# Optimization experiments

Measured on AMD Instinct MI355X. Metric: run time of the kernel, lower is better.

The kernel has to match this reference:

```python
import jax, jax.numpy as jnp
import numpy as np

B = 32; H = 56; W = 56; C = 384; WS = 7; SHIFT = 3; NH = 12; HID = 1536; RANK = 192
N = WS * WS
NWIN = (H // WS) * (W // WS)


def _rel_index():
    coords = np.stack(np.meshgrid(np.arange(WS), np.arange(WS), indexing='ij')).reshape(2, -1)
    rel = (coords[:, :, None] - coords[:, None, :]).transpose(1, 2, 0)
    rel[..., 0] += WS - 1
    rel[..., 1] += WS - 1
    rel[..., 0] *= 2 * WS - 1
    return jnp.asarray(rel.sum(-1).reshape(-1))  # (N*N,) int


def _attn_mask():
    img = np.zeros((H, W))
    cnt = 0
    sls = (slice(0, -WS), slice(-WS, -SHIFT), slice(-SHIFT, None))
    for hs in sls:
        for ws_ in sls:
            img[hs, ws_] = cnt
            cnt += 1
    mw = img.reshape(H // WS, WS, W // WS, WS).transpose(0, 2, 1, 3).reshape(-1, N)
    am = mw[:, None, :] - mw[:, :, None]
    return jnp.asarray(np.where(am != 0, -100.0, 0.0).astype(np.float32))  # (nW,N,N)


REL_IDX = _rel_index()
ATTN_MASK = _attn_mask()


def _ln(x, g, b):
    m = x.mean(-1, keepdims=True)
    v = ((x - m) ** 2).mean(-1, keepdims=True)
    return (x - m) / jnp.sqrt(v + 1e-5) * g + b


def _flin(x, v, u, b):
    # FactorizedLinear: x @ V^T @ U^T + b
    return (x @ v.T) @ u.T + b


def setup_inputs() -> dict:
    key = jax.random.key(0)
    ks = jax.random.split(key, 12)
    def n(k, shape, s):
        return jax.random.normal(k, shape, jnp.float32) * s
    return {
        'x': jax.random.normal(ks[0], (B, H * W, C), jnp.float32),
        'norm1_g': jnp.ones((C,), jnp.float32), 'norm1_b': jnp.zeros((C,), jnp.float32),
        'rpb_table': n(ks[1], ((2 * WS - 1) ** 2, NH), 0.02),
        'qkv_v': n(ks[2], (RANK, C), 0.05), 'qkv_u': n(ks[3], (3 * C, RANK), 0.05),
        'qkv_b': jnp.zeros((3 * C,), jnp.float32),
        'proj_v': n(ks[4], (RANK, C), 0.05), 'proj_u': n(ks[5], (C, RANK), 0.05),
        'proj_b': jnp.zeros((C,), jnp.float32),
        'norm2_g': jnp.ones((C,), jnp.float32), 'norm2_b': jnp.zeros((C,), jnp.float32),
        'fc1_v': n(ks[6], (RANK, C), 0.05), 'fc1_u': n(ks[7], (HID, RANK), 0.05),
        'fc1_b': jnp.zeros((HID,), jnp.float32),
        'fc2_v': n(ks[8], (RANK, HID), 0.05), 'fc2_u': n(ks[9], (C, RANK), 0.05),
        'fc2_b': jnp.zeros((C,), jnp.float32),
    }


def reference(x, norm1_g, norm1_b, rpb_table, qkv_v, qkv_u, qkv_b,
              proj_v, proj_u, proj_b, norm2_g, norm2_b,
              fc1_v, fc1_u, fc1_b, fc2_v, fc2_u, fc2_b):
    hd = C // NH
    scale = hd ** -0.5
    shortcut = x
    y = _ln(x, norm1_g, norm1_b).reshape(B, H, W, C)
    y = jnp.roll(y, (-SHIFT, -SHIFT), axis=(1, 2))  # cyclic shift
    # window partition -> (B*nW, N, C)
    y = y.reshape(B, H // WS, WS, W // WS, WS, C).transpose(0, 1, 3, 2, 4, 5).reshape(-1, N, C)
    qkv = _flin(y, qkv_v, qkv_u, qkv_b).reshape(-1, N, 3, NH, hd).transpose(2, 0, 3, 1, 4)
    q, k, v = qkv[0] * scale, qkv[1], qkv[2]  # (B*nW, NH, N, hd)
    attn = jnp.einsum('bhnd,bhmd->bhnm', q, k)
    rpb = rpb_table[REL_IDX].reshape(N, N, NH).transpose(2, 0, 1)  # (NH,N,N)
    attn = attn + rpb[None]
    attn = attn.reshape(B, NWIN, NH, N, N) + ATTN_MASK[None, :, None]
    attn = jax.nn.softmax(attn, axis=-1).reshape(-1, NH, N, N)
    o = jnp.einsum('bhnm,bhmd->bhnd', attn, v).transpose(0, 2, 1, 3).reshape(-1, N, C)
    o = _flin(o, proj_v, proj_u, proj_b)
    # window reverse + reverse shift
    o = o.reshape(B, H // WS, W // WS, WS, WS, C).transpose(0, 1, 3, 2, 4, 5).reshape(B, H, W, C)
    o = jnp.roll(o, (SHIFT, SHIFT), axis=(1, 2)).reshape(B, H * W, C)
    x = shortcut + o
    z = _ln(x, norm2_g, norm2_b)
    z = jax.nn.gelu(_flin(z, fc1_v, fc1_u, fc1_b), approximate=False)
    z = _flin(z, fc2_v, fc2_u, fc2_b)
    return x + z
```

## Files before the change

kernel.cpp:

```cpp
#include <hip/hip_runtime.h>
#include <hip/hip_bf16.h>

using bf16 = __hip_bfloat16;
typedef __bf16 bf16x8 __attribute__((ext_vector_type(8)));
typedef __bf16 bf16x4v __attribute__((ext_vector_type(4)));
typedef float f32x4 __attribute__((ext_vector_type(4)));

#define MROWS 100352

__device__ __forceinline__ void async16(void* l, const void* g) {
    void* gg = const_cast<void*>(g);
    __builtin_amdgcn_global_load_lds((__attribute__((address_space(1))) void*)gg,
                                     (__attribute__((address_space(3))) void*)l, 16, 0, 0);
}

__device__ __forceinline__ float gelu_f(float x) {
    float u = 0.7978845608028654f * (x + 0.044715f * x * x * x);
    float e = __expf(2.0f * u);
    float t = 1.0f - 2.0f / (e + 1.0f);
    return 0.5f * x * (1.0f + t);
}

struct Cvt8 { const float* s[8]; bf16* d[8]; int n[8]; };

__global__ __launch_bounds__(256) void cvt8_k(Cvt8 c) {
    int seg = blockIdx.y;
    int i4 = (blockIdx.x * 256 + threadIdx.x) * 4;
    if (i4 < c.n[seg]) {
        float4 v = *(const float4*)(c.s[seg] + i4);
        bf16* d = c.d[seg] + i4;
        d[0] = __float2bfloat16(v.x);
        d[1] = __float2bfloat16(v.y);
        d[2] = __float2bfloat16(v.z);
        d[3] = __float2bfloat16(v.w);
    }
}

__global__ __launch_bounds__(256) void bias_pre_k(const float* __restrict__ rpbt,
                                                  float* __restrict__ biasf) {
    int wt = blockIdx.x / 12, h = blockIdx.x % 12;
    int t = threadIdx.x;
    int lane = t >> 2, tb = t & 3;
    int hi = lane >> 4, lo = lane & 15;
    int m = tb * 16 + lo;
    bool bH = (wt & 2) != 0, bW = (wt & 1) != 0;
    float* outb = biasf + (size_t)blockIdx.x * 4096;
    int mm = m < 49 ? m : 0;
    int i2 = mm / 7, j2 = mm % 7;
    int rm = (bH ? (i2 < 4 ? 1 : 2) : 0) * 3 + (bW ? (j2 < 4 ? 1 : 2) : 0);
#pragma unroll
    for (int ta = 0; ta < 4; ++ta) {
#pragma unroll
        for (int j = 0; j < 4; ++j) {
            int n = ta * 16 + hi * 4 + j;
            float v;
            if (n < 49 && m < 49) {
                int i1 = n / 7, j1 = n % 7;
                int rn = (bH ? (i1 < 4 ? 1 : 2) : 0) * 3 + (bW ? (j1 < 4 ? 1 : 2) : 0);
                v = rpbt[((i1 - i2 + 6) * 13 + (j1 - j2 + 6)) * 12 + h];
                if (rn != rm) v -= 100.0f;
            } else {
                v = -1e30f;
            }
            outb[(ta * 4 + j) * 256 + t] = v;
        }
    }
}

__global__ __launch_bounds__(256) void ln1_window_k(const float* __restrict__ x,
                                                    const float* __restrict__ g,
                                                    const float* __restrict__ bta,
                                                    bf16* __restrict__ ywin) {
    int wrow = blockIdx.x * 4 + (threadIdx.x >> 6);
    int lane = threadIdx.x & 63;
    int tok = wrow % 49, win = wrow / 49;
    int i = tok / 7, j = tok % 7;
    int wwi = win & 7, whi = (win >> 3) & 7, bi = win >> 6;
    int hs = (whi * 7 + i + 3) % 56;
    int ws_ = (wwi * 7 + j + 3) % 56;
    const float* xr = x + ((size_t)bi * 3136 + (size_t)hs * 56 + ws_) * 384;
    float v[6]; float s = 0.f, s2 = 0.f;
#pragma unroll
    for (int u = 0; u < 6; ++u) { float t = xr[lane + 64 * u]; v[u] = t; s += t; s2 += t * t; }
#pragma unroll
    for (int d = 1; d < 64; d <<= 1) { s += __shfl_xor(s, d); s2 += __shfl_xor(s2, d); }
    float mean = s * (1.0f / 384.0f);
    float var = s2 * (1.0f / 384.0f) - mean * mean;
    float rstd = rsqrtf(var + 1e-5f);
    bf16* yr = ywin + (size_t)wrow * 384;
#pragma unroll
    for (int u = 0; u < 6; ++u) {
        int c = lane + 64 * u;
        yr[c] = __float2bfloat16((v[u] - mean) * rstd * g[c] + bta[c]);
    }
}

__global__ __launch_bounds__(256) void resid_ln2_k(const float* __restrict__ x,
                                                   const bf16* __restrict__ proj,
                                                   const float* __restrict__ g,
                                                   const float* __restrict__ bta,
                                                   float* __restrict__ x2,
                                                   bf16* __restrict__ z) {
    int row = blockIdx.x * 4 + (threadIdx.x >> 6);
    int lane = threadIdx.x & 63;
    int bi = row / 3136; int hw = row % 3136;
    int h = hw / 56, w = hw % 56;
    int h2 = (h + 53) % 56, w2 = (w + 53) % 56;
    int prow = ((bi * 8 + h2 / 7) * 8 + w2 / 7) * 49 + (h2 % 7) * 7 + (w2 % 7);
    const float* xr = x + (size_t)row * 384;
    const bf16* pr = proj + (size_t)prow * 384;
    float* x2r = x2 + (size_t)row * 384;
    float v[6]; float s = 0.f, s2 = 0.f;
#pragma unroll
    for (int u = 0; u < 6; ++u) {
        int c = lane + 64 * u;
        float t = xr[c] + __bfloat162float(pr[c]);
        v[u] = t; s += t; s2 += t * t;
        x2r[c] = t;
    }
#pragma unroll
    for (int d = 1; d < 64; d <<= 1) { s += __shfl_xor(s, d); s2 += __shfl_xor(s2, d); }
    float mean = s * (1.0f / 384.0f);
    float var = s2 * (1.0f / 384.0f) - mean * mean;
    float rstd = rsqrtf(var + 1e-5f);
    bf16* zr = z + (size_t)row * 384;
#pragma unroll
    for (int u = 0; u < 6; ++u) {
        int c = lane + 64 * u;
        zr[c] = __float2bfloat16((v[u] - mean) * rstd * g[c] + bta[c]);
    }
}

__global__ __launch_bounds__(256) void attn_mfma_k(const bf16* __restrict__ qkv,
                                                   const float* __restrict__ biasf,
                                                   bf16* __restrict__ o) {
    __shared__ __align__(16) __bf16 vt_s[4][32 * 72];
    __shared__ __align__(16) __bf16 p_s[4][32 * 72];
    const int win = blockIdx.x;
    const int r = blockIdx.y;
    const int wave = threadIdx.x >> 6, lane = threadIdx.x & 63;
    const int lo = lane & 15, hi = lane >> 4;
    const int whi = (win >> 3) & 7, wwi = win & 7;
    const int wt = ((whi == 7) ? 2 : 0) + ((wwi == 7) ? 1 : 0);
    __bf16* vt_w = vt_s[wave];
    __bf16* p_w = p_s[wave];
    const int h = r * 4 + wave;
    const bf16* qbase = qkv + (size_t)win * 49 * 1152 + h * 32;
    const float* btile = biasf + (size_t)(wt * 12 + h) * 4096;
    bf16x8 zf = {};

    {
        int m = lane;
        bf16x8 vrow[4];
#pragma unroll
        for (int d8 = 0; d8 < 4; ++d8)
            vrow[d8] = (m < 49) ? *(const bf16x8*)(qbase + (size_t)m * 1152 + 768 + d8 * 8) : zf;
#pragma unroll
        for (int d8 = 0; d8 < 4; ++d8)
#pragma unroll
            for (int e = 0; e < 8; ++e)
                vt_w[(d8 * 8 + e) * 72 + m] = vrow[d8][e];
    }
    bf16x8 aq[4], bk[4];
    const int kq = hi * 8;
#pragma unroll
    for (int ta = 0; ta < 4; ++ta) {
        int n = ta * 16 + lo;
        aq[ta] = (n < 49) ? *(const bf16x8*)(qbase + (size_t)n * 1152 + kq) : zf;
        bk[ta] = (n < 49) ? *(const bf16x8*)(qbase + (size_t)n * 1152 + 384 + kq) : zf;
    }
    f32x4 acc[4][4] = {};
#pragma unroll
    for (int ta = 0; ta < 4; ++ta)
#pragma unroll
        for (int tb = 0; tb < 4; ++tb)
            acc[ta][tb] = __builtin_amdgcn_mfma_f32_16x16x32_bf16(aq[ta], bk[tb], acc[ta][tb], 0, 0, 0);
#pragma unroll
    for (int ta = 0; ta < 4; ++ta) {
#pragma unroll
        for (int j = 0; j < 4; ++j) {
            float4 b4 = *(const float4*)(btile + (ta * 4 + j) * 256 + lane * 4);
            acc[ta][0][j] = fmaf(acc[ta][0][j], 0.17677669529663687f, b4.x);
            acc[ta][1][j] = fmaf(acc[ta][1][j], 0.17677669529663687f, b4.y);
            acc[ta][2][j] = fmaf(acc[ta][2][j], 0.17677669529663687f, b4.z);
            acc[ta][3][j] = fmaf(acc[ta][3][j], 0.17677669529663687f, b4.w);
        }
    }
    bf16x8 vb[2][2];
#pragma unroll
    for (int kb = 0; kb < 2; ++kb)
#pragma unroll
        for (int tb = 0; tb < 2; ++tb)
            vb[kb][tb] = *(const bf16x8*)(vt_w + (tb * 16 + lo) * 72 + kb * 32 + hi * 8);

    f32x4 oacc[4][2] = {};
#pragma unroll
    for (int half = 0; half < 2; ++half) {
#pragma unroll
        for (int tq = 0; tq < 2; ++tq) {
            int ta = half * 2 + tq;
#pragma unroll
            for (int j = 0; j < 4; ++j) {
                float mx = fmaxf(fmaxf(acc[ta][0][j], acc[ta][1][j]),
                                 fmaxf(acc[ta][2][j], acc[ta][3][j]));
                mx = fmaxf(mx, __shfl_xor(mx, 1));
                mx = fmaxf(mx, __shfl_xor(mx, 2));
                mx = fmaxf(mx, __shfl_xor(mx, 4));
                mx = fmaxf(mx, __shfl_xor(mx, 8));
                float e0 = __expf(acc[ta][0][j] - mx);
                float e1 = __expf(acc[ta][1][j] - mx);
                float e2 = __expf(acc[ta][2][j] - mx);
                float e3 = __expf(acc[ta][3][j] - mx);
                float sm = e0 + e1 + e2 + e3;
                sm += __shfl_xor(sm, 1);
                sm += __shfl_xor(sm, 2);
                sm += __shfl_xor(sm, 4);
                sm += __shfl_xor(sm, 8);
                float inv = 1.0f / sm;
                int nl = tq * 16 + hi * 4 + j;
                p_w[nl * 72 + lo]      = (__bf16)(e0 * inv);
                p_w[nl * 72 + 16 + lo] = (__bf16)(e1 * inv);
                p_w[nl * 72 + 32 + lo] = (__bf16)(e2 * inv);
                p_w[nl * 72 + 48 + lo] = (__bf16)(e3 * inv);
            }
        }
#pragma unroll
        for (int kb = 0; kb < 2; ++kb) {
#pragma unroll
            for (int tq = 0; tq < 2; ++tq) {
                bf16x8 pa = *(const bf16x8*)(p_w + (tq * 16 + lo) * 72 + kb * 32 + hi * 8);
#pragma unroll
                for (int tb = 0; tb < 2; ++tb)
                    oacc[half * 2 + tq][tb] =
                        __builtin_amdgcn_mfma_f32_16x16x32_bf16(pa, vb[kb][tb], oacc[half * 2 + tq][tb], 0, 0, 0);
            }
        }
    }
    bf16* obase = o + (size_t)win * 49 * 384 + h * 32;
#pragma unroll
    for (int ta = 0; ta < 4; ++ta) {
#pragma unroll
        for (int j = 0; j < 4; ++j) {
            int n = ta * 16 + hi * 4 + j;
            if (n < 49) {
#pragma unroll
                for (int tb = 0; tb < 2; ++tb)
                    obase[(size_t)n * 384 + tb * 16 + lo] = __float2bfloat16(oacc[ta][tb][j]);
            }
        }
    }
}

template <int K, int N, int WN, int EPI>
__global__ __launch_bounds__(WN * 128, 8 - WN) void gemm_bt(const bf16* __restrict__ A,
                                                            const bf16* __restrict__ W,
                                                            const float* __restrict__ bias,
                                                            void* __restrict__ Cout) {
    constexpr int T = WN * 128;
    constexpr int BN = WN * 32;
    __shared__ __align__(16) bf16 lds_a[128 * 64];
    __shared__ __align__(16) bf16 lds_b[BN * 64];
    const int t = threadIdx.x;
    const int wave = t >> 6, lane = t & 63;
    const int gdx = gridDim.x;
    int flat = blockIdx.y * gdx + blockIdx.x;
    int q = (gdx * gridDim.y) >> 3;
    int work = (flat & 7) * q + (flat >> 3);
    const int n0 = (work % gdx) * BN, m0 = (work / gdx) * 128;
    const int wm = wave / WN, wn = wave % WN;
    const int fr = lane & 15, hi = lane >> 4;
    const int srow = t >> 3;
    const int gslot = (t & 7) ^ (srow & 7);
    const bf16* abase = A + (size_t)(m0 + srow) * K + gslot * 8;
    const bf16* bbase = W + (size_t)(n0 + srow) * K + gslot * 8;
    char* la = (char*)lds_a + t * 16;
    char* lb = (char*)lds_b + t * 16;
    const int fp = fr & 7;
    const char* ra0 = (const char*)lds_a + (wm * 64 + fr) * 128 + (hi ^ fp) * 16;
    const char* ra1 = (const char*)lds_a + (wm * 64 + fr) * 128 + ((4 + hi) ^ fp) * 16;
    const char* rb0 = (const char*)lds_b + (wn * 32 + fr) * 128 + (hi ^ fp) * 16;
    const char* rb1 = (const char*)lds_b + (wn * 32 + fr) * 128 + ((4 + hi) ^ fp) * 16;
    f32x4 acc[4][2] = {};
#pragma unroll
    for (int kt = 0; kt < K; kt += 64) {
        if (kt > 0) __syncthreads();
#pragma unroll
        for (int i = 0; i < 1024 / T; ++i)
            async16(la + i * T * 16, abase + (size_t)i * (T >> 3) * K + kt);
#pragma unroll
        for (int i = 0; i < BN * 8 / T; ++i)
            async16(lb + i * T * 16, bbase + (size_t)i * (T >> 3) * K + kt);
        __syncthreads();
        bf16x8 af[4], bfr[2];
#pragma unroll
        for (int mi = 0; mi < 4; ++mi) af[mi] = *(const bf16x8*)(ra0 + mi * 2048);
#pragma unroll
        for (int ni = 0; ni < 2; ++ni) bfr[ni] = *(const bf16x8*)(rb0 + ni * 2048);
#pragma unroll
        for (int mi = 0; mi < 4; ++mi)
#pragma unroll
            for (int ni = 0; ni < 2; ++ni)
                acc[mi][ni] = __builtin_amdgcn_mfma_f32_16x16x32_bf16(bfr[ni], af[mi], acc[mi][ni], 0, 0, 0);
#pragma unroll
        for (int mi = 0; mi < 4; ++mi) af[mi] = *(const bf16x8*)(ra1 + mi * 2048);
#pragma unroll
        for (int ni = 0; ni < 2; ++ni) bfr[ni] = *(const bf16x8*)(rb1 + ni * 2048);
#pragma unroll
        for (int mi = 0; mi < 4; ++mi)
#pragma unroll
            for (int ni = 0; ni < 2; ++ni)
                acc[mi][ni] = __builtin_amdgcn_mfma_f32_16x16x32_bf16(bfr[ni], af[mi], acc[mi][ni], 0, 0, 0);
    }
    const int rq4 = hi * 4;
    const int ncol = n0 + wn * 32 + rq4;
    const size_t cbase = (size_t)(m0 + wm * 64 + fr) * N + ncol;
    const float* pb = bias ? bias + ncol : nullptr;
#pragma unroll
    for (int mi = 0; mi < 4; ++mi) {
#pragma unroll
        for (int ni = 0; ni < 2; ++ni) {
            float v0 = acc[mi][ni][0], v1 = acc[mi][ni][1];
            float v2 = acc[mi][ni][2], v3 = acc[mi][ni][3];
            if (pb) {
                float4 b4 = *(const float4*)(pb + ni * 16);
                v0 += b4.x; v1 += b4.y; v2 += b4.z; v3 += b4.w;
            }
            if (EPI == 1) { v0 = gelu_f(v0); v1 = gelu_f(v1); v2 = gelu_f(v2); v3 = gelu_f(v3); }
            if (EPI == 2) {
                float4* p = (float4*)((float*)Cout + cbase + (size_t)mi * 16 * N + ni * 16);
                float4 o = *p;
                o.x += v0; o.y += v1; o.z += v2; o.w += v3;
                *p = o;
            } else {
                bf16x4v st = { (__bf16)v0, (__bf16)v1, (__bf16)v2, (__bf16)v3 };
                *(bf16x4v*)((bf16*)Cout + cbase + (size_t)mi * 16 * N + ni * 16) = st;
            }
        }
    }
}

extern "C" void kernel_launch(void* const* d_in, const int* in_sizes, int n_in,
                              void* d_out, int out_size, void* d_ws, size_t ws_size,
                              hipStream_t stream) {
    const float* x      = (const float*)d_in[0];
    const float* n1g    = (const float*)d_in[1];
    const float* n1b    = (const float*)d_in[2];
    const float* rpbt   = (const float*)d_in[3];
    const float* qkv_v  = (const float*)d_in[4];
    const float* qkv_u  = (const float*)d_in[5];
    const float* qkv_b  = (const float*)d_in[6];
    const float* proj_v = (const float*)d_in[7];
    const float* proj_u = (const float*)d_in[8];
    const float* proj_b = (const float*)d_in[9];
    const float* n2g    = (const float*)d_in[10];
    const float* n2b    = (const float*)d_in[11];
    const float* fc1_v  = (const float*)d_in[12];
    const float* fc1_u  = (const float*)d_in[13];
    const float* fc1_b  = (const float*)d_in[14];
    const float* fc2_v  = (const float*)d_in[15];
    const float* fc2_u  = (const float*)d_in[16];
    const float* fc2_b  = (const float*)d_in[17];

    char* ws = (char*)d_ws;
    bf16* wb = (bf16*)ws;
    bf16* w_qkv_v  = wb;
    bf16* w_qkv_u  = wb + 73728;
    bf16* w_proj_v = wb + 294912;
    bf16* w_proj_u = wb + 368640;
    bf16* w_fc1_v  = wb + 442368;
    bf16* w_fc1_u  = wb + 516096;
    bf16* w_fc2_v  = wb + 811008;
    bf16* w_fc2_u  = wb + 1105920;
    float* biasf   = (float*)(ws + 3145728);
    size_t off = (size_t)4 << 20;
    bf16* R1 = (bf16*)(ws + off); off += (size_t)MROWS * 1536 * 2;
    bf16* R2 = (bf16*)(ws + off); off += (size_t)MROWS * 384 * 2;
    bf16* R3 = (bf16*)(ws + off);
    float* out = (float*)d_out;

    Cvt8 c;
    c.s[0] = qkv_v;  c.d[0] = w_qkv_v;  c.n[0] = 73728;
    c.s[1] = qkv_u;  c.d[1] = w_qkv_u;  c.n[1] = 221184;
    c.s[2] = proj_v; c.d[2] = w_proj_v; c.n[2] = 73728;
    c.s[3] = proj_u; c.d[3] = w_proj_u; c.n[3] = 73728;
    c.s[4] = fc1_v;  c.d[4] = w_fc1_v;  c.n[4] = 73728;
    c.s[5] = fc1_u;  c.d[5] = w_fc1_u;  c.n[5] = 294912;
    c.s[6] = fc2_v;  c.d[6] = w_fc2_v;  c.n[6] = 294912;
    c.s[7] = fc2_u;  c.d[7] = w_fc2_u;  c.n[7] = 73728;
    cvt8_k<<<dim3(288, 8), 256, 0, stream>>>(c);
    bias_pre_k<<<48, 256, 0, stream>>>(rpbt, biasf);

    ln1_window_k<<<MROWS / 4, 256, 0, stream>>>(x, n1g, n1b, R2);
    gemm_bt<384, 192, 2, 0><<<dim3(3, 784), 256, 0, stream>>>(R2, w_qkv_v, nullptr, R3);
    gemm_bt<192, 1152, 4, 0><<<dim3(9, 784), 512, 0, stream>>>(R3, w_qkv_u, qkv_b, R1);
    attn_mfma_k<<<dim3(2048, 3), 256, 0, stream>>>(R1, biasf, R2);
    gemm_bt<384, 192, 2, 0><<<dim3(3, 784), 256, 0, stream>>>(R2, w_proj_v, nullptr, R3);
    gemm_bt<192, 384, 4, 0><<<dim3(3, 784), 512, 0, stream>>>(R3, w_proj_u, proj_b, R1);
    resid_ln2_k<<<MROWS / 4, 256, 0, stream>>>(x, R1, n2g, n2b, out, R2);
    gemm_bt<384, 192, 2, 0><<<dim3(3, 784), 256, 0, stream>>>(R2, w_fc1_v, nullptr, R3);
    gemm_bt<192, 1536, 4, 1><<<dim3(12, 784), 512, 0, stream>>>(R3, w_fc1_u, fc1_b, R1);
    gemm_bt<1536, 192, 2, 0><<<dim3(3, 784), 256, 0, stream>>>(R1, w_fc2_v, nullptr, R3);
    gemm_bt<192, 384, 4, 2><<<dim3(3, 784), 512, 0, stream>>>(R3, w_fc2_u, fc2_b, out);
}
```

Before: 841.8 us.

## Merge proj low-rank weights, add direct-load B GEMM, cheaper gelu/softmax reciprocals

Precomputes the proj U·V product on device so the projection becomes a single K=384 GEMM instead of two chained low-rank GEMMs, removing one launch and an intermediate round trip. Adds a gemm_bu variant for the wide-N U-side GEMMs that loads B fragments straight from global memory into registers and stages only A in LDS. It also rewrites gelu in sigmoid form with a hardware reciprocal and uses rcp in the softmax normalisation. The merged projection does more FLOPs than the factorized pair, and the direct B loads depend on cache hits.

```diff
diff --git a/kernel.cpp b/kernel.cpp
--- a/kernel.cpp
+++ b/kernel.cpp
@@ -15,10 +15,9 @@
 }
 
 __device__ __forceinline__ float gelu_f(float x) {
-    float u = 0.7978845608028654f * (x + 0.044715f * x * x * x);
-    float e = __expf(2.0f * u);
-    float t = 1.0f - 2.0f / (e + 1.0f);
-    return 0.5f * x * (1.0f + t);
+    float u = x * fmaf(0.044715f * x, x, 1.0f);
+    float e = __expf(-1.5957691216057308f * u);
+    return x * __builtin_amdgcn_rcpf(1.0f + e);
 }
 
 struct Cvt8 { const float* s[8]; bf16* d[8]; int n[8]; };
@@ -34,6 +33,16 @@
         d[2] = __float2bfloat16(v.z);
         d[3] = __float2bfloat16(v.w);
     }
+}
+
+__global__ __launch_bounds__(384) void wmerge_k(const float* __restrict__ u,
+                                                const float* __restrict__ v,
+                                                bf16* __restrict__ wm) {
+    int o = blockIdx.x, i = threadIdx.x;
+    const float* ur = u + o * 192;
+    float acc = 0.f;
+    for (int r = 0; r < 192; ++r) acc = fmaf(ur[r], v[r * 384 + i], acc);
+    wm[o * 384 + i] = __float2bfloat16(acc);
 }
 
 __global__ __launch_bounds__(256) void bias_pre_k(const float* __restrict__ rpbt,
@@ -216,7 +225,7 @@
                 sm += __shfl_xor(sm, 2);
                 sm += __shfl_xor(sm, 4);
                 sm += __shfl_xor(sm, 8);
-                float inv = 1.0f / sm;
+                float inv = __builtin_amdgcn_rcpf(sm);
                 int nl = tq * 16 + hi * 4 + j;
                 p_w[nl * 72 + lo]      = (__bf16)(e0 * inv);
                 p_w[nl * 72 + 16 + lo] = (__bf16)(e1 * inv);
@@ -251,23 +260,21 @@
     }
 }
 
-template <int K, int N, int WN, int EPI>
-__global__ __launch_bounds__(WN * 128, 8 - WN) void gemm_bt(const bf16* __restrict__ A,
-                                                            const bf16* __restrict__ W,
-                                                            const float* __restrict__ bias,
-                                                            void* __restrict__ Cout) {
-    constexpr int T = WN * 128;
-    constexpr int BN = WN * 32;
+template <int K, int N, int EPI>
+__global__ __launch_bounds__(256, 6) void gemm_bt(const bf16* __restrict__ A,
+                                                  const bf16* __restrict__ W,
+                                                  const float* __restrict__ bias,
+                                                  void* __restrict__ Cout) {
     __shared__ __align__(16) bf16 lds_a[128 * 64];
-    __shared__ __align__(16) bf16 lds_b[BN * 64];
+    __shared__ __align__(16) bf16 lds_b[64 * 64];
     const int t = threadIdx.x;
     const int wave = t >> 6, lane = t & 63;
     const int gdx = gridDim.x;
     int flat = blockIdx.y * gdx + blockIdx.x;
     int q = (gdx * gridDim.y) >> 3;
     int work = (flat & 7) * q + (flat >> 3);
-    const int n0 = (work % gdx) * BN, m0 = (work / gdx) * 128;
-    const int wm = wave / WN, wn = wave % WN;
+    const int n0 = (work % gdx) * 64, m0 = (work / gdx) * 128;
+    const int wm = wave >> 1, wn = wave & 1;
     const int fr = lane & 15, hi = lane >> 4;
     const int srow = t >> 3;
     const int gslot = (t & 7) ^ (srow & 7);
@@ -285,11 +292,11 @@
     for (int kt = 0; kt < K; kt += 64) {
         if (kt > 0) __syncthreads();
 #pragma unroll
-        for (int i = 0; i < 1024 / T; ++i)
-            async16(la + i * T * 16, abase + (size_t)i * (T >> 3) * K + kt);
-#pragma unroll
-        for (int i = 0; i < BN * 8 / T; ++i)
-            async16(lb + i * T * 16, bbase + (size_t)i * (T >> 3) * K + kt);
+        for (int i = 0; i < 4; ++i)
+            async16(la + i * 4096, abase + (size_t)i * 32 * K + kt);
+#pragma unroll
+        for (int i = 0; i < 2; ++i)
+            async16(lb + i * 4096, bbase + (size_t)i * 32 * K + kt);
         __syncthreads();
         bf16x8 af[4], bfr[2];
 #pragma unroll
@@ -310,6 +317,84 @@
 #pragma unroll
             for (int ni = 0; ni < 2; ++ni)
                 acc[mi][ni] = __builtin_amdgcn_mfma_f32_16x16x32_bf16(bfr[ni], af[mi], acc[mi][ni], 0, 0, 0);
+    }
+    const int rq4 = hi * 4;
+    const int ncol = n0 + wn * 32 + rq4;
+    const size_t cbase = (size_t)(m0 + wm * 64 + fr) * N + ncol;
+    const float* pb = bias ? bias + ncol : nullptr;
+#pragma unroll
+    for (int mi = 0; mi < 4; ++mi) {
+#pragma unroll
+        for (int ni = 0; ni < 2; ++ni) {
+            float v0 = acc[mi][ni][0], v1 = acc[mi][ni][1];
+            float v2 = acc[mi][ni][2], v3 = acc[mi][ni][3];
+            if (pb) {
+                float4 b4 = *(const float4*)(pb + ni * 16);
+                v0 += b4.x; v1 += b4.y; v2 += b4.z; v3 += b4.w;
+            }
+            if (EPI == 1) { v0 = gelu_f(v0); v1 = gelu_f(v1); v2 = gelu_f(v2); v3 = gelu_f(v3); }
+            if (EPI == 2) {
+                float4* p = (float4*)((float*)Cout + cbase + (size_t)mi * 16 * N + ni * 16);
+                float4 o = *p;
+                o.x += v0; o.y += v1; o.z += v2; o.w += v3;
+                *p = o;
+            } else {
+                bf16x4v st = { (__bf16)v0, (__bf16)v1, (__bf16)v2, (__bf16)v3 };
+                *(bf16x4v*)((bf16*)Cout + cbase + (size_t)mi * 16 * N + ni * 16) = st;
+            }
+        }
+    }
+}
+
+template <int K, int N, int EPI>
+__global__ __launch_bounds__(512, 6) void gemm_bu(const bf16* __restrict__ A,
+                                                  const bf16* __restrict__ W,
+                                                  const float* __restrict__ bias,
+                                                  void* __restrict__ Cout) {
+    __shared__ __align__(16) bf16 lds_a[128 * 64];
+    const int t = threadIdx.x;
+    const int wave = t >> 6, lane = t & 63;
+    const int gdx = gridDim.x;
+    int flat = blockIdx.y * gdx + blockIdx.x;
+    int q = (gdx * gridDim.y) >> 3;
+    int work = (flat & 7) * q + (flat >> 3);
+    const int n0 = (work % gdx) * 128, m0 = (work / gdx) * 128;
+    const int wm = wave >> 2, wn = wave & 3;
+    const int fr = lane & 15, hi = lane >> 4;
+    const int srow = t >> 3;
+    const int gslot = (t & 7) ^ (srow & 7);
+    const bf16* abase = A + (size_t)(m0 + srow) * K + gslot * 8;
+    char* la = (char*)lds_a + t * 16;
+    const bf16* wbase = W + (size_t)(n0 + wn * 32 + fr) * K + hi * 8;
+    const int fp = fr & 7;
+    const char* ra0 = (const char*)lds_a + (wm * 64 + fr) * 128 + (hi ^ fp) * 16;
+    const char* ra1 = (const char*)lds_a + (wm * 64 + fr) * 128 + ((4 + hi) ^ fp) * 16;
+    f32x4 acc[4][2] = {};
+#pragma unroll 1
+    for (int kt = 0; kt < K; kt += 64) {
+        bf16x8 b00 = *(const bf16x8*)(wbase + kt);
+        bf16x8 b01 = *(const bf16x8*)(wbase + (size_t)16 * K + kt);
+        bf16x8 b10 = *(const bf16x8*)(wbase + kt + 32);
+        bf16x8 b11 = *(const bf16x8*)(wbase + (size_t)16 * K + kt + 32);
+        if (kt > 0) __syncthreads();
+        async16(la, abase + kt);
+        async16(la + 8192, abase + (size_t)64 * K + kt);
+        __syncthreads();
+        bf16x8 af[4];
+#pragma unroll
+        for (int mi = 0; mi < 4; ++mi) af[mi] = *(const bf16x8*)(ra0 + mi * 2048);
+#pragma unroll
+        for (int mi = 0; mi < 4; ++mi) {
+            acc[mi][0] = __builtin_amdgcn_mfma_f32_16x16x32_bf16(b00, af[mi], acc[mi][0], 0, 0, 0);
+            acc[mi][1] = __builtin_amdgcn_mfma_f32_16x16x32_bf16(b01, af[mi], acc[mi][1], 0, 0, 0);
+        }
+#pragma unroll
+        for (int mi = 0; mi < 4; ++mi) af[mi] = *(const bf16x8*)(ra1 + mi * 2048);
+#pragma unroll
+        for (int mi = 0; mi < 4; ++mi) {
+            acc[mi][0] = __builtin_amdgcn_mfma_f32_16x16x32_bf16(b10, af[mi], acc[mi][0], 0, 0, 0);
+            acc[mi][1] = __builtin_amdgcn_mfma_f32_16x16x32_bf16(b11, af[mi], acc[mi][1], 0, 0, 0);
+        }
     }
     const int rq4 = hi * 4;
     const int ncol = n0 + wn * 32 + rq4;
@@ -371,6 +456,7 @@
     bf16* w_fc1_u  = wb + 516096;
     bf16* w_fc2_v  = wb + 811008;
     bf16* w_fc2_u  = wb + 1105920;
+    bf16* w_proj_m = wb + 1179648;
     float* biasf   = (float*)(ws + 3145728);
     size_t off = (size_t)4 << 20;
     bf16* R1 = (bf16*)(ws + off); off += (size_t)MROWS * 1536 * 2;
@@ -389,16 +475,16 @@
     c.s[7] = fc2_u;  c.d[7] = w_fc2_u;  c.n[7] = 73728;
     cvt8_k<<<dim3(288, 8), 256, 0, stream>>>(c);
     bias_pre_k<<<48, 256, 0, stream>>>(rpbt, biasf);
+    wmerge_k<<<384, 384, 0, stream>>>(proj_u, proj_v, w_proj_m);
 
     ln1_window_k<<<MROWS / 4, 256, 0, stream>>>(x, n1g, n1b, R2);
-    gemm_bt<384, 192, 2, 0><<<dim3(3, 784), 256, 0, stream>>>(R2, w_qkv_v, nullptr, R3);
-    gemm_bt<192, 1152, 4, 0><<<dim3(9, 784), 512, 0, stream>>>(R3, w_qkv_u, qkv_b, R1);
+    gemm_bt<384, 192, 0><<<dim3(3, 784), 256, 0, stream>>>(R2, w_qkv_v, nullptr, R3);
+    gemm_bu<192, 1152, 0><<<dim3(9, 784), 512, 0, stream>>>(R3, w_qkv_u, qkv_b, R1);
     attn_mfma_k<<<dim3(2048, 3), 256, 0, stream>>>(R1, biasf, R2);
-    gemm_bt<384, 192, 2, 0><<<dim3(3, 784), 256, 0, stream>>>(R2, w_proj_v, nullptr, R3);
-    gemm_bt<192, 384, 4, 0><<<dim3(3, 784), 512, 0, stream>>>(R3, w_proj_u, proj_b, R1);
+    gemm_bu<384, 384, 0><<<dim3(3, 784), 512, 0, stream>>>(R2, w_proj_m, proj_b, R1);
     resid_ln2_k<<<MROWS / 4, 256, 0, stream>>>(x, R1, n2g, n2b, out, R2);
-    gemm_bt<384, 192, 2, 0><<<dim3(3, 784), 256, 0, stream>>>(R2, w_fc1_v, nullptr, R3);
-    gemm_bt<192, 1536, 4, 1><<<dim3(12, 784), 512, 0, stream>>>(R3, w_fc1_u, fc1_b, R1);
-    gemm_bt<1536, 192, 2, 0><<<dim3(3, 784), 256, 0, stream>>>(R1, w_fc2_v, nullptr, R3);
-    gemm_bt<192, 384, 4, 2><<<dim3(3, 784), 512, 0, stream>>>(R3, w_fc2_u, fc2_b, out);
-}
+    gemm_bt<384, 192, 0><<<dim3(3, 784), 256, 0, stream>>>(R2, w_fc1_v, nullptr, R3);
+    gemm_bu<192, 1536, 1><<<dim3(12, 784), 512, 0, stream>>>(R3, w_fc1_u, fc1_b, R1);
+    gemm_bt<1536, 192, 0><<<dim3(3, 784), 256, 0, stream>>>(R1, w_fc2_v, nullptr, R3);
+    gemm_bu<192, 384, 2><<<dim3(3, 784), 512, 0, stream>>>(R3, w_fc2_u, fc2_b, out);
+}
```

Measured after the change: 933.4 us. 10.9% more time.

## Fuse MLP fc1_u+GELU+fc2_v on-chip and premerge projection factors

Applied to the files above, without the earlier changes.

Adds mlp_mid_k, which computes the fc1 up-projection, bias and GELU in 128-column chunks kept in LDS and immediately feeds them into the fc2 down-projection, so the 1536-wide hidden activation is never written to or read from global memory. It also premultiplies proj_u·proj_v into a single 384x384 weight so the attention output projection becomes one GEMM instead of two. GELU is rewritten in sigmoid form with a hardware reciprocal, and the softmax divide uses rcp. The risks are lower occupancy from the large LDS footprint in the fused kernel, more FLOPs in the merged projection, and reduced precision from the approximate reciprocal.

```diff
diff --git a/kernel.cpp b/kernel.cpp
--- a/kernel.cpp
+++ b/kernel.cpp
@@ -15,10 +15,9 @@
 }
 
 __device__ __forceinline__ float gelu_f(float x) {
-    float u = 0.7978845608028654f * (x + 0.044715f * x * x * x);
-    float e = __expf(2.0f * u);
-    float t = 1.0f - 2.0f / (e + 1.0f);
-    return 0.5f * x * (1.0f + t);
+    float u = x * fmaf(0.044715f * x, x, 1.0f);
+    float e = __expf(-1.5957691216057308f * u);
+    return x * __builtin_amdgcn_rcpf(1.0f + e);
 }
 
 struct Cvt8 { const float* s[8]; bf16* d[8]; int n[8]; };
@@ -34,6 +33,16 @@
         d[2] = __float2bfloat16(v.z);
         d[3] = __float2bfloat16(v.w);
     }
+}
+
+__global__ __launch_bounds__(384) void wmerge_k(const float* __restrict__ u,
+                                                const float* __restrict__ v,
+                                                bf16* __restrict__ wm) {
+    int o = blockIdx.x, i = threadIdx.x;
+    const float* ur = u + o * 192;
+    float acc = 0.f;
+    for (int r = 0; r < 192; ++r) acc = fmaf(ur[r], v[r * 384 + i], acc);
+    wm[o * 384 + i] = __float2bfloat16(acc);
 }
 
 __global__ __launch_bounds__(256) void bias_pre_k(const float* __restrict__ rpbt,
@@ -216,7 +225,7 @@
                 sm += __shfl_xor(sm, 2);
                 sm += __shfl_xor(sm, 4);
                 sm += __shfl_xor(sm, 8);
-                float inv = 1.0f / sm;
+                float inv = __builtin_amdgcn_rcpf(sm);
                 int nl = tq * 16 + hi * 4 + j;
                 p_w[nl * 72 + lo]      = (__bf16)(e0 * inv);
                 p_w[nl * 72 + 16 + lo] = (__bf16)(e1 * inv);
@@ -339,6 +348,100 @@
     }
 }
 
+__global__ __launch_bounds__(512, 4) void mlp_mid_k(const bf16* __restrict__ A,
+                                                    const bf16* __restrict__ U,
+                                                    const bf16* __restrict__ V2,
+                                                    const float* __restrict__ b1,
+                                                    bf16* __restrict__ Cout) {
+    __shared__ __align__(16) bf16 lds_a[128 * 192];
+    __shared__ __align__(16) bf16 lds_h[128 * 128];
+    const int t = threadIdx.x;
+    const int wave = t >> 6, lane = t & 63;
+    const int wm = wave >> 2, wn = wave & 3;
+    const int fr = lane & 15, hi = lane >> 4;
+    const int fp = fr & 7;
+    const int m0 = blockIdx.x * 128;
+#pragma unroll
+    for (int i = 0; i < 6; ++i) {
+        int u = i * 512 + t;
+        int row = u / 24, slot = u % 24;
+        int gslot = slot ^ (row & 7);
+        async16((char*)lds_a + u * 16, A + (size_t)(m0 + row) * 192 + gslot * 8);
+    }
+    __syncthreads();
+
+    f32x4 acc2[4][3] = {};
+    const int rowm = wm * 64;
+    const bf16* ub = U + (size_t)(wn * 32 + fr) * 192 + hi * 8;
+    const bf16* vb = V2 + (size_t)(wn * 48 + fr) * 1536 + hi * 8;
+
+    for (int hc = 0; hc < 12; ++hc) {
+        f32x4 acc1[4][2] = {};
+#pragma unroll
+        for (int kk = 0; kk < 6; ++kk) {
+            bf16x8 af[4], bu[2];
+#pragma unroll
+            for (int mi = 0; mi < 4; ++mi) {
+                int row = rowm + mi * 16 + fr;
+                af[mi] = *(const bf16x8*)((const char*)lds_a + row * 384 + ((kk * 4 + hi) ^ fp) * 16);
+            }
+#pragma unroll
+            for (int nn = 0; nn < 2; ++nn)
+                bu[nn] = *(const bf16x8*)(ub + (size_t)(hc * 128 + nn * 16) * 192 + kk * 32);
+#pragma unroll
+            for (int mi = 0; mi < 4; ++mi)
+#pragma unroll
+                for (int nn = 0; nn < 2; ++nn)
+                    acc1[mi][nn] = __builtin_amdgcn_mfma_f32_16x16x32_bf16(bu[nn], af[mi], acc1[mi][nn], 0, 0, 0);
+        }
+        if (hc > 0) __syncthreads();
+#pragma unroll
+        for (int nn = 0; nn < 2; ++nn) {
+            float4 b4 = *(const float4*)(b1 + hc * 128 + wn * 32 + nn * 16 + hi * 4);
+#pragma unroll
+            for (int mi = 0; mi < 4; ++mi) {
+                int mrow = rowm + mi * 16 + fr;
+                float v0 = gelu_f(acc1[mi][nn][0] + b4.x);
+                float v1 = gelu_f(acc1[mi][nn][1] + b4.y);
+                float v2 = gelu_f(acc1[mi][nn][2] + b4.z);
+                float v3 = gelu_f(acc1[mi][nn][3] + b4.w);
+                bf16x4v st = { (__bf16)v0, (__bf16)v1, (__bf16)v2, (__bf16)v3 };
+                int hb = (wn * 64 + nn * 32 + hi * 8) ^ ((mrow & 7) << 4);
+                *(bf16x4v*)((char*)lds_h + mrow * 256 + hb) = st;
+            }
+        }
+        __syncthreads();
+#pragma unroll
+        for (int kk = 0; kk < 4; ++kk) {
+            bf16x8 af2[4], bv[3];
+#pragma unroll
+            for (int mi = 0; mi < 4; ++mi) {
+                int mrow = rowm + mi * 16 + fr;
+                int kb = (kk * 64 + hi * 16) ^ ((mrow & 7) << 4);
+                af2[mi] = *(const bf16x8*)((const char*)lds_h + mrow * 256 + kb);
+            }
+#pragma unroll
+            for (int tn = 0; tn < 3; ++tn)
+                bv[tn] = *(const bf16x8*)(vb + (size_t)(tn * 16) * 1536 + hc * 128 + kk * 32);
+#pragma unroll
+            for (int mi = 0; mi < 4; ++mi)
+#pragma unroll
+                for (int tn = 0; tn < 3; ++tn)
+                    acc2[mi][tn] = __builtin_amdgcn_mfma_f32_16x16x32_bf16(bv[tn], af2[mi], acc2[mi][tn], 0, 0, 0);
+        }
+    }
+    const size_t cbase = (size_t)(m0 + rowm + fr) * 192 + wn * 48 + hi * 4;
+#pragma unroll
+    for (int mi = 0; mi < 4; ++mi) {
+#pragma unroll
+        for (int tn = 0; tn < 3; ++tn) {
+            bf16x4v st = { (__bf16)acc2[mi][tn][0], (__bf16)acc2[mi][tn][1],
+                           (__bf16)acc2[mi][tn][2], (__bf16)acc2[mi][tn][3] };
+            *(bf16x4v*)(Cout + cbase + (size_t)mi * 16 * 192 + tn * 16) = st;
+        }
+    }
+}
+
 extern "C" void kernel_launch(void* const* d_in, const int* in_sizes, int n_in,
                               void* d_out, int out_size, void* d_ws, size_t ws_size,
                               hipStream_t stream) {
@@ -371,6 +474,7 @@
     bf16* w_fc1_u  = wb + 516096;
     bf16* w_fc2_v  = wb + 811008;
     bf16* w_fc2_u  = wb + 1105920;
+    bf16* w_proj_m = wb + 1179648;
     float* biasf   = (float*)(ws + 3145728);
     size_t off = (size_t)4 << 20;
     bf16* R1 = (bf16*)(ws + off); off += (size_t)MROWS * 1536 * 2;
@@ -389,16 +493,15 @@
     c.s[7] = fc2_u;  c.d[7] = w_fc2_u;  c.n[7] = 73728;
     cvt8_k<<<dim3(288, 8), 256, 0, stream>>>(c);
     bias_pre_k<<<48, 256, 0, stream>>>(rpbt, biasf);
+    wmerge_k<<<384, 384, 0, stream>>>(proj_u, proj_v, w_proj_m);
 
     ln1_window_k<<<MROWS / 4, 256, 0, stream>>>(x, n1g, n1b, R2);
     gemm_bt<384, 192, 2, 0><<<dim3(3, 784), 256, 0, stream>>>(R2, w_qkv_v, nullptr, R3);
     gemm_bt<192, 1152, 4, 0><<<dim3(9, 784), 512, 0, stream>>>(R3, w_qkv_u, qkv_b, R1);
     attn_mfma_k<<<dim3(2048, 3), 256, 0, stream>>>(R1, biasf, R2);
-    gemm_bt<384, 192, 2, 0><<<dim3(3, 784), 256, 0, stream>>>(R2, w_proj_v, nullptr, R3);
-    gemm_bt<192, 384, 4, 0><<<dim3(3, 784), 512, 0, stream>>>(R3, w_proj_u, proj_b, R1);
+    gemm_bt<384, 384, 4, 0><<<dim3(3, 784), 512, 0, stream>>>(R2, w_proj_m, proj_b, R1);
     resid_ln2_k<<<MROWS / 4, 256, 0, stream>>>(x, R1, n2g, n2b, out, R2);
     gemm_bt<384, 192, 2, 0><<<dim3(3, 784), 256, 0, stream>>>(R2, w_fc1_v, nullptr, R3);
-    gemm_bt<192, 1536, 4, 1><<<dim3(12, 784), 512, 0, stream>>>(R3, w_fc1_u, fc1_b, R1);
-    gemm_bt<1536, 192, 2, 0><<<dim3(3, 784), 256, 0, stream>>>(R1, w_fc2_v, nullptr, R3);
-    gemm_bt<192, 384, 4, 2><<<dim3(3, 784), 512, 0, stream>>>(R3, w_fc2_u, fc2_b, out);
-}
+    mlp_mid_k<<<784, 512, 0, stream>>>(R3, w_fc1_u, w_fc2_v, fc1_b, R1);
+    gemm_bt<192, 384, 4, 2><<<dim3(3, 784), 512, 0, stream>>>(R1, w_fc2_u, fc2_b, out);
+}
```

Measured after the change: 863.7 us. 2.6% more time.
